# Performance work log

Hardware: AMD Instinct MI355X
Metric: run time of the kernel (lower is better)

The kernel has to match this reference:

```python
import jax, jax.numpy as jnp
import numpy as np

B, T1, T2, D = 8, 2048, 2048, 256


def setup_inputs() -> dict:
    key = jax.random.key(0)
    k1, k2 = jax.random.split(key)
    s1 = jax.random.normal(k1, (B, T1, D), dtype=jnp.float32)
    s2 = jax.random.normal(k2, (B, T2, D), dtype=jnp.float32)
    return {"s1": s1, "s2": s2}


def reference(s1, s2):
    # similarity: [B, t1, t2]
    s = jnp.einsum('bid,bjd->bij', s1, s2)
    # softmax over t2, replace NaNs with 0 (matches masked_fill_(w != w, 0))
    w = jax.nn.softmax(s, axis=2)
    w = jnp.where(jnp.isnan(w), jnp.zeros((), w.dtype), w)
    # one-hot of argmax over t2 (vectorized replacement of the double loop)
    idx = jnp.argmax(w, axis=2)                       # [B, t1]
    a_weight_like = jax.nn.one_hot(idx, s2.shape[1], dtype=s1.dtype)  # [B, t1, t2]
    # gather the argmax rows of s2: [B, t1, D]
    u_tile = jnp.einsum('bij,bjd->bid', a_weight_like, s2)
    return (u_tile, a_weight_like)
```

## Files before the change

kernel.cpp:

```cpp
#include <hip/hip_runtime.h>
#include <math.h>

typedef unsigned short ushort_t;

constexpr int BB = 8, T1 = 2048, T2 = 2048, D = 256;
constexpr float MARGIN = 4e-3f;

constexpr size_t OFF_QC    = 0;
constexpr size_t OFF_QUEUE = 64;
constexpr size_t OFF_PART  = 131072;
constexpr size_t OFF_S1P   = (size_t)2 << 20;
constexpr size_t SZ_PACK   = (size_t)BB * 128 * 8 * 2 * 64 * 16;
constexpr size_t OFF_S2P   = OFF_S1P + SZ_PACK;
constexpr size_t WS_NEEDED = OFF_S2P + SZ_PACK;

typedef __attribute__((ext_vector_type(8))) __bf16 bf16x8;
typedef __attribute__((ext_vector_type(4))) float  f32x4;

__device__ __forceinline__ unsigned f2bf(float x) {
    unsigned u = __float_as_uint(x);
    return (u + 0x7fffu + ((u >> 16) & 1u)) >> 16;
}
__device__ __forceinline__ float bf2f(unsigned h) { return __uint_as_float(h << 16); }

__global__ __launch_bounds__(256) void k_convert(
    const float* __restrict__ s1, const float* __restrict__ s2,
    ushort_t* __restrict__ s1p, ushort_t* __restrict__ s2p)
{
    __shared__ __align__(16) ushort_t L[16384];
    const int bx = blockIdx.x;
    const int tensor = bx >> 9, b = (bx >> 6) & 7, rt = bx & 63;
    const float* src = (tensor ? s2 : s1) + ((size_t)b * 2048 + rt * 32) * 256;
    ushort_t* dst = (tensor ? s2p : s1p) + (size_t)(b * 128 + rt * 2) * 8192;
    const int t = threadIdx.x;
#pragma unroll
    for (int i = 0; i < 8; ++i) {
        int f = i * 256 + t, rw = f >> 6, c4 = f & 63, k0 = c4 * 4;
        float4 v = *(const float4*)(src + rw * 256 + k0);
        unsigned hx = f2bf(v.x), hy = f2bf(v.y), hz = f2bf(v.z), hw = f2bf(v.w);
        ushort4 hi = make_ushort4((ushort_t)hx, (ushort_t)hy, (ushort_t)hz, (ushort_t)hw);
        ushort4 lo = make_ushort4((ushort_t)f2bf(v.x - bf2f(hx)), (ushort_t)f2bf(v.y - bf2f(hy)),
                                  (ushort_t)f2bf(v.z - bf2f(hz)), (ushort_t)f2bf(v.w - bf2f(hw)));
        int tile = rw >> 4, m = rw & 15, g = k0 >> 5;
        int lane = m + 16 * ((k0 >> 3) & 3), i0 = k0 & 7;
        int off = (tile * 8 + g) * 1024 + lane * 8 + i0;
        *(ushort4*)(&L[off])       = hi;
        *(ushort4*)(&L[off + 512]) = lo;
    }
    __syncthreads();
#pragma unroll
    for (int i = 0; i < 8; ++i) {
        int cidx = i * 256 + t;
        ((uint4*)dst)[cidx] = ((const uint4*)L)[cidx];
    }
}

__global__ __launch_bounds__(256, 2) void k_score(
    const ushort_t* __restrict__ s1p, const ushort_t* __restrict__ s2p,
    float4* __restrict__ part)
{
    __shared__ __align__(16) ushort_t AL[16 * 512];
    __shared__ __align__(16) ushort_t BL[32 * 512];
    __shared__ float4 mrg[128][2];

    const int bx = blockIdx.x;
    const int b = bx & 7, rt16 = (bx >> 3) & 15, jq = bx >> 7;
    const int t = threadIdx.x, w = t >> 6, l = t & 63;
    const int rh = w >> 1, jw = w & 1;
    const int q = l >> 4, n = l & 15;

    mrg[t >> 1][t & 1] = make_float4(-INFINITY, -INFINITY, __int_as_float(0), 0.f);

    const ushort_t* Abase = s1p + (size_t)(b * 128 + rt16 * 8) * 8192;

    f32x4 acc[4][8];

    for (int jiter = 0; jiter < 2; ++jiter) {
        const ushort_t* Bbase = s2p + (size_t)(b * 128 + jq * 32 + jiter * 16) * 8192;
#pragma unroll
        for (int rtl = 0; rtl < 4; ++rtl)
#pragma unroll
            for (int jt = 0; jt < 8; ++jt)
#pragma unroll
                for (int r = 0; r < 4; ++r) acc[rtl][jt][r] = 0.f;

        for (int g = 0; g < 8; ++g) {
            __syncthreads();
            for (int s = 0; s * 4 < 48; ++s) {
                int c = s * 4 + w;
                uint4 v;
                if (c < 16)
                    v = *(const uint4*)(Abase + (size_t)(c >> 1) * 8192 + g * 1024 + (c & 1) * 512 + l * 8);
                else {
                    int cc = c - 16;
                    v = *(const uint4*)(Bbase + (size_t)(cc >> 1) * 8192 + g * 1024 + (cc & 1) * 512 + l * 8);
                }
                if (c < 16) *(uint4*)(&AL[c * 512 + l * 8]) = v;
                else        *(uint4*)(&BL[(c - 16) * 512 + l * 8]) = v;
            }
            __syncthreads();

            bf16x8 aF[4][2];
#pragma unroll
            for (int rtl = 0; rtl < 4; ++rtl)
#pragma unroll
                for (int lb = 0; lb < 2; ++lb)
                    aF[rtl][lb] = *(const bf16x8*)(&AL[((rh * 4 + rtl) * 2 + lb) * 512 + l * 8]);
#pragma unroll
            for (int jt = 0; jt < 8; ++jt) {
                bf16x8 bh = *(const bf16x8*)(&BL[((jw * 8 + jt) * 2 + 0) * 512 + l * 8]);
                bf16x8 bl = *(const bf16x8*)(&BL[((jw * 8 + jt) * 2 + 1) * 512 + l * 8]);
#pragma unroll
                for (int rtl = 0; rtl < 4; ++rtl) {
                    acc[rtl][jt] = __builtin_amdgcn_mfma_f32_16x16x32_bf16(aF[rtl][0], bh, acc[rtl][jt], 0, 0, 0);
                    acc[rtl][jt] = __builtin_amdgcn_mfma_f32_16x16x32_bf16(aF[rtl][0], bl, acc[rtl][jt], 0, 0, 0);
                    acc[rtl][jt] = __builtin_amdgcn_mfma_f32_16x16x32_bf16(aF[rtl][1], bh, acc[rtl][jt], 0, 0, 0);
                }
            }
        }

#pragma unroll
        for (int rtl = 0; rtl < 4; ++rtl)
#pragma unroll
            for (int reg = 0; reg < 4; ++reg) {
                float v1 = -INFINITY, v2 = -INFINITY; int i1 = 0;
#pragma unroll
                for (int jt = 0; jt < 8; ++jt) {
                    float v = acc[rtl][jt][reg];
                    int j = jq * 512 + jiter * 256 + jw * 128 + jt * 16 + n;
                    if (v > v1)      { v2 = v1; v1 = v; i1 = j; }
                    else if (v > v2) { v2 = v; }
                }
#pragma unroll
                for (int off = 1; off < 16; off <<= 1) {
                    float b1 = __shfl_xor(v1, off);
                    int   bi = __shfl_xor(i1, off);
                    float b2 = __shfl_xor(v2, off);
                    if (b1 > v1 || (b1 == v1 && bi < i1)) { v2 = fmaxf(v1, b2); v1 = b1; i1 = bi; }
                    else                                   { v2 = fmaxf(b1, v2); }
                }
                int rr = rtl * 4 + reg;
                if (n == rr) {
                    int row = rh * 64 + rtl * 16 + q * 4 + reg;
                    float4 cur = mrg[row][jw];
                    int ci = __float_as_int(cur.z);
                    if (v1 > cur.x || (v1 == cur.x && i1 < ci))
                        mrg[row][jw] = make_float4(v1, fmaxf(v2, cur.x), __int_as_float(i1), 0.f);
                    else
                        mrg[row][jw] = make_float4(cur.x, fmaxf(cur.y, v1), cur.z, 0.f);
                }
            }
    }

    __syncthreads();
    if (t < 128) {
        float4 p0 = mrg[t][0], p1 = mrg[t][1];
        int i0 = __float_as_int(p0.z), i1 = __float_as_int(p1.z);
        float v1, v2; int ii;
        if (p1.x > p0.x || (p1.x == p0.x && i1 < i0)) { v1 = p1.x; v2 = fmaxf(p1.y, p0.x); ii = i1; }
        else                                          { v1 = p0.x; v2 = fmaxf(p0.y, p1.x); ii = i0; }
        part[((size_t)b * 2048 + rt16 * 128 + t) * 4 + jq] =
            make_float4(v1, v2, __int_as_float(ii), 0.f);
    }
}

__global__ __launch_bounds__(256) void k_epilogue(
    const float* __restrict__ s2, const float4* __restrict__ part,
    float* __restrict__ u, float* __restrict__ oh,
    int* __restrict__ qcount, int* __restrict__ queue)
{
    __shared__ int idxs[8];
    const int blk = blockIdx.x, t = threadIdx.x;
    const int r0 = blk * 8;
    const int b = r0 >> 11;
    if (t < 32) {
        int rl = t >> 2, p = t & 3;
        float4 pa = part[(size_t)(r0 + rl) * 4 + p];
        float v1 = pa.x, v2 = pa.y; int i1 = __float_as_int(pa.z);
#pragma unroll
        for (int off = 1; off < 4; off <<= 1) {
            float b1 = __shfl_xor(v1, off);
            int   bi = __shfl_xor(i1, off);
            float b2 = __shfl_xor(v2, off);
            if (b1 > v1 || (b1 == v1 && bi < i1)) { v2 = fmaxf(v1, b2); v1 = b1; i1 = bi; }
            else                                   { v2 = fmaxf(b1, v2); }
        }
        if (p == 0) {
            idxs[rl] = i1;
            if ((v1 - v2) < MARGIN) {
                int pos = atomicAdd(qcount, 1);
                if (pos < 16384) queue[pos] = r0 + rl;
            }
        }
    }
    __syncthreads();
    const float* s2b = s2 + (size_t)b * T2 * D;
    float* ub = u + (size_t)r0 * D;
#pragma unroll
    for (int i = 0; i < 2; ++i) {
        int flat = i * 256 + t, rl = flat >> 6, c = flat & 63;
        float4 v = *(const float4*)(s2b + (size_t)idxs[rl] * D + c * 4);
        *(float4*)(ub + (size_t)rl * D + c * 4) = v;
    }
    float* ohb = oh + (size_t)r0 * T2;
#pragma unroll 4
    for (int i = 0; i < 16; ++i) {
        int flat = i * 256 + t, rl = flat >> 9, c4 = flat & 511;
        int base = c4 * 4, id = idxs[rl];
        float4 vv;
        vv.x = (base     == id) ? 1.f : 0.f;
        vv.y = (base + 1 == id) ? 1.f : 0.f;
        vv.z = (base + 2 == id) ? 1.f : 0.f;
        vv.w = (base + 3 == id) ? 1.f : 0.f;
        *(float4*)(ohb + (size_t)rl * T2 + base) = vv;
    }
}

__global__ __launch_bounds__(256) void k_fixup(
    const float* __restrict__ s1, const float* __restrict__ s2,
    float* __restrict__ u, float* __restrict__ oh,
    const int* __restrict__ qcount, const int* __restrict__ queue, int qcap)
{
    __shared__ double s1d[D];
    __shared__ double rv[256];
    __shared__ int    rj[256];
    int nq = *qcount;
    if (nq > qcap) nq = qcap;
    const int t = threadIdx.x;
    for (int qi = blockIdx.x; qi < nq; qi += gridDim.x) {
        int rg = queue[qi];
        int b = rg >> 11, i = rg & (T1 - 1);
        __syncthreads();
        s1d[t] = (double)s1[((size_t)b * T1 + i) * D + t];
        __syncthreads();
        double bv = -INFINITY; int bj = 0;
        for (int jj = 0; jj < T2 / 256; ++jj) {
            int j = t + jj * 256;
            const float* row = s2 + ((size_t)b * T2 + j) * D;
            double s = 0.0;
            for (int k = 0; k < D; ++k) s = fma((double)row[k], s1d[k], s);
            if (s > bv) { bv = s; bj = j; }
        }
        rv[t] = bv; rj[t] = bj;
        __syncthreads();
        for (int stride = 128; stride > 0; stride >>= 1) {
            if (t < stride) {
                double ov = rv[t + stride]; int oj = rj[t + stride];
                if (ov > rv[t] || (ov == rv[t] && oj < rj[t])) { rv[t] = ov; rj[t] = oj; }
            }
            __syncthreads();
        }
        int best = rj[0];
        float* ohrow = oh + ((size_t)b * T1 + i) * T2;
#pragma unroll
        for (int jj = 0; jj < T2 / 256; ++jj) {
            int j = t + jj * 256;
            ohrow[j] = (j == best) ? 1.f : 0.f;
        }
        u[((size_t)b * T1 + i) * D + t] = s2[((size_t)b * T2 + best) * D + t];
    }
}

constexpr int FB_AST = 264, FB_BST = 72;

__global__ __launch_bounds__(512, 2) void k_score_fb(
    const float* __restrict__ s1, const float* __restrict__ s2,
    float* __restrict__ u, float* __restrict__ oh,
    int* __restrict__ qcount, int* __restrict__ queue, int qcap)
{
    __shared__ __align__(16) short Ah[64 * FB_AST];
    __shared__ __align__(16) short Al[64 * FB_AST];
    __shared__ __align__(16) short Bh[256 * FB_BST];
    __shared__ __align__(16) short Bl[256 * FB_BST];
    __shared__ float cv1[64][4], cv2[64][4];
    __shared__ int   ci1[64][4], idx_s[64];

    const int bx = blockIdx.x;
    const int b  = bx & 7;
    const int r0 = (bx >> 3) * 64;
    const float* s1b = s1 + ((size_t)b * T1 + r0) * D;
    const float* s2b = s2 + (size_t)b * T2 * D;

    const int t = threadIdx.x;
    const int w = t >> 6, l = t & 63, q = l >> 4, ln = l & 15;
    const int rh = w >> 2;
    const int jq = w & 3;

    float4 pa[8];
#pragma unroll
    for (int i = 0; i < 8; ++i) {
        int flat = i * 512 + t, row = flat >> 6, f4 = flat & 63;
        pa[i] = *(const float4*)(s1b + row * D + f4 * 4);
    }
    float4 pb[8];
#pragma unroll
    for (int i = 0; i < 8; ++i) {
        int flat = i * 512 + t, jrow = flat >> 4, f4 = flat & 15;
        pb[i] = *(const float4*)(s2b + (size_t)jrow * D + f4 * 4);
    }
#pragma unroll
    for (int i = 0; i < 8; ++i) {
        int flat = i * 512 + t, row = flat >> 6, f4 = flat & 63;
        float4 v = pa[i];
        unsigned hx = f2bf(v.x), hy = f2bf(v.y), hz = f2bf(v.z), hw = f2bf(v.w);
        uint2 hh, ll;
        hh.x = hx | (hy << 16); hh.y = hz | (hw << 16);
        ll.x = f2bf(v.x - bf2f(hx)) | (f2bf(v.y - bf2f(hy)) << 16);
        ll.y = f2bf(v.z - bf2f(hz)) | (f2bf(v.w - bf2f(hw)) << 16);
        *(uint2*)(&Ah[row * FB_AST + f4 * 4]) = hh;
        *(uint2*)(&Al[row * FB_AST + f4 * 4]) = ll;
    }

    float v1[2][4], v2[2][4]; int i1[2][4];
#pragma unroll
    for (int rt = 0; rt < 2; ++rt)
#pragma unroll
        for (int r = 0; r < 4; ++r) { v1[rt][r] = -INFINITY; v2[rt][r] = -INFINITY; i1[rt][r] = 0; }

    f32x4 acc[2][4];

    for (int c = 0; c < 32; ++c) {
        const int iter = c >> 2, kc = c & 3;
        if (kc == 0) {
#pragma unroll
            for (int rt = 0; rt < 2; ++rt)
#pragma unroll
                for (int jt = 0; jt < 4; ++jt)
#pragma unroll
                    for (int r = 0; r < 4; ++r) acc[rt][jt][r] = 0.f;
        }
        __syncthreads();
#pragma unroll
        for (int i = 0; i < 8; ++i) {
            int flat = i * 512 + t, jrow = flat >> 4, f4 = flat & 15;
            float4 v = pb[i];
            unsigned hx = f2bf(v.x), hy = f2bf(v.y), hz = f2bf(v.z), hw = f2bf(v.w);
            uint2 hh, ll;
            hh.x = hx | (hy << 16); hh.y = hz | (hw << 16);
            ll.x = f2bf(v.x - bf2f(hx)) | (f2bf(v.y - bf2f(hy)) << 16);
            ll.y = f2bf(v.z - bf2f(hz)) | (f2bf(v.w - bf2f(hw)) << 16);
            *(uint2*)(&Bh[jrow * FB_BST + f4 * 4]) = hh;
            *(uint2*)(&Bl[jrow * FB_BST + f4 * 4]) = ll;
        }
        if (c < 31) {
            int c2 = c + 1, it2 = c2 >> 2, kc2 = c2 & 3;
#pragma unroll
            for (int i = 0; i < 8; ++i) {
                int flat = i * 512 + t, jrow = flat >> 4, f4 = flat & 15;
                pb[i] = *(const float4*)(s2b + (size_t)(it2 * 256 + jrow) * D + kc2 * 64 + f4 * 4);
            }
        }
        __syncthreads();

#pragma unroll
        for (int ks = 0; ks < 2; ++ks) {
            const int kA = kc * 64 + ks * 32 + q * 8;
            bf16x8 ah[2], al8[2];
#pragma unroll
            for (int rt = 0; rt < 2; ++rt) {
                int off = (rh * 32 + rt * 16 + ln) * FB_AST + kA;
                ah[rt]  = *(const bf16x8*)(&Ah[off]);
                al8[rt] = *(const bf16x8*)(&Al[off]);
            }
#pragma unroll
            for (int jt = 0; jt < 4; ++jt) {
                int boff = (jq * 64 + jt * 16 + ln) * FB_BST + ks * 32 + q * 8;
                bf16x8 bh = *(const bf16x8*)(&Bh[boff]);
                bf16x8 bl = *(const bf16x8*)(&Bl[boff]);
#pragma unroll
                for (int rt = 0; rt < 2; ++rt) {
                    acc[rt][jt] = __builtin_amdgcn_mfma_f32_16x16x32_bf16(ah[rt],  bh, acc[rt][jt], 0, 0, 0);
                    acc[rt][jt] = __builtin_amdgcn_mfma_f32_16x16x32_bf16(ah[rt],  bl, acc[rt][jt], 0, 0, 0);
                    acc[rt][jt] = __builtin_amdgcn_mfma_f32_16x16x32_bf16(al8[rt], bh, acc[rt][jt], 0, 0, 0);
                }
            }
        }

        if (kc == 3) {
#pragma unroll
            for (int rt = 0; rt < 2; ++rt)
#pragma unroll
                for (int jt = 0; jt < 4; ++jt)
#pragma unroll
                    for (int r = 0; r < 4; ++r) {
                        float val = acc[rt][jt][r];
                        int j = iter * 256 + jq * 64 + jt * 16 + ln;
                        if (val > v1[rt][r]) { v2[rt][r] = v1[rt][r]; v1[rt][r] = val; i1[rt][r] = j; }
                        else if (val > v2[rt][r]) v2[rt][r] = val;
                    }
        }
    }

#pragma unroll
    for (int rt = 0; rt < 2; ++rt)
#pragma unroll
        for (int r = 0; r < 4; ++r) {
            float a1 = v1[rt][r], a2 = v2[rt][r]; int ai = i1[rt][r];
#pragma unroll
            for (int off = 1; off < 16; off <<= 1) {
                float b1 = __shfl_xor(a1, off);
                int   bi = __shfl_xor(ai, off);
                float b2 = __shfl_xor(a2, off);
                if (b1 > a1 || (b1 == a1 && bi < ai)) { a2 = fmaxf(a1, b2); a1 = b1; ai = bi; }
                else                                   { a2 = fmaxf(b1, a2); }
            }
            if (ln == 0) {
                int row = rh * 32 + rt * 16 + q * 4 + r;
                cv1[row][jq] = a1; cv2[row][jq] = a2; ci1[row][jq] = ai;
            }
        }
    __syncthreads();

    if (t < 64) {
        float V1 = cv1[t][0], V2 = cv2[t][0]; int I = ci1[t][0];
#pragma unroll
        for (int h = 1; h < 4; ++h) {
            float c1 = cv1[t][h], c2 = cv2[t][h]; int ci = ci1[t][h];
            if (c1 > V1 || (c1 == V1 && ci < I)) { V2 = fmaxf(V1, c2); V1 = c1; I = ci; }
            else                                  { V2 = fmaxf(V2, c1); }
        }
        idx_s[t] = I;
        if (qcap > 0 && (V1 - V2) < MARGIN) {
            int pos = atomicAdd(qcount, 1);
            if (pos < qcap) queue[pos] = b * T1 + r0 + t;
        }
    }
    __syncthreads();

    float* ub = u + ((size_t)b * T1 + r0) * D;
#pragma unroll
    for (int i = 0; i < 8; ++i) {
        int flat = i * 512 + t, row = flat >> 6, f4 = flat & 63;
        float4 v = *(const float4*)(s2b + (size_t)idx_s[row] * D + f4 * 4);
        *(float4*)(ub + (size_t)row * D + f4 * 4) = v;
    }
    float* ohb = oh + ((size_t)b * T1 + r0) * T2;
#pragma unroll 4
    for (int i = 0; i < 64; ++i) {
        int flat = i * 512 + t, row = flat >> 9, f4 = flat & 511;
        int base = f4 * 4, id = idx_s[row];
        float4 vv;
        vv.x = (base     == id) ? 1.f : 0.f;
        vv.y = (base + 1 == id) ? 1.f : 0.f;
        vv.z = (base + 2 == id) ? 1.f : 0.f;
        vv.w = (base + 3 == id) ? 1.f : 0.f;
        *(float4*)(ohb + (size_t)row * T2 + base) = vv;
    }
}

extern "C" void kernel_launch(void* const* d_in, const int* in_sizes, int n_in,
                              void* d_out, int out_size, void* d_ws, size_t ws_size,
                              hipStream_t stream)
{
    const float* s1 = (const float*)d_in[0];
    const float* s2 = (const float*)d_in[1];
    float* u  = (float*)d_out;
    float* oh = u + (size_t)BB * T1 * D;
    char* ws = (char*)d_ws;

    if (ws_size >= WS_NEEDED) {
        int*      qc    = (int*)(ws + OFF_QC);
        int*      queue = (int*)(ws + OFF_QUEUE);
        float4*   part  = (float4*)(ws + OFF_PART);
        ushort_t* s1p   = (ushort_t*)(ws + OFF_S1P);
        ushort_t* s2p   = (ushort_t*)(ws + OFF_S2P);
        hipMemsetAsync(ws + OFF_QC, 0, 16, stream);
        k_convert<<<dim3(1024), dim3(256), 0, stream>>>(s1, s2, s1p, s2p);
        k_score<<<dim3(512), dim3(256), 0, stream>>>(s1p, s2p, part);
        k_epilogue<<<dim3(2048), dim3(256), 0, stream>>>(s2, part, u, oh, qc, queue);
        k_fixup<<<dim3(128), dim3(256), 0, stream>>>(s1, s2, u, oh, qc, queue, 16384);
    } else {
        int  qcap   = 0;
        int* qcount = nullptr;
        int* queue  = nullptr;
        if (ws_size >= 256) {
            qcount = (int*)d_ws;
            queue  = (int*)d_ws + 4;
            size_t cap = (ws_size - 16) / sizeof(int);
            qcap = (int)(cap > (size_t)(BB * T1) ? (size_t)(BB * T1) : cap);
            hipMemsetAsync(d_ws, 0, 16, stream);
        }
        k_score_fb<<<dim3(BB * (T1 / 64)), dim3(512), 0, stream>>>(
            s1, s2, u, oh, qcount, queue, qcap);
        if (qcap > 0)
            k_fixup<<<dim3(64), dim3(256), 0, stream>>>(
                s1, s2, u, oh, qcount, queue, qcap);
    }
}
```

Before: 312.8 us.

## Load MFMA fragments directly from global memory instead of staging through LDS

The score kernel no longer stages A and B tiles into shared memory with two barriers per k-step. Each wave now reads its bf16 fragments straight from the pre-packed global buffers, relying on L2/L1 caching for reuse between waves. This drops LDS traffic and barrier stalls, but each A tile is now fetched by two waves and each B tile by two waves from global/cache. Global load latency is also exposed unless the compiler overlaps it with the MFMAs.

```diff
diff --git a/kernel.cpp b/kernel.cpp
--- a/kernel.cpp
+++ b/kernel.cpp
@@ -59,8 +59,6 @@
     const ushort_t* __restrict__ s1p, const ushort_t* __restrict__ s2p,
     float4* __restrict__ part)
 {
-    __shared__ __align__(16) ushort_t AL[16 * 512];
-    __shared__ __align__(16) ushort_t BL[32 * 512];
     __shared__ float4 mrg[128][2];
 
     const int bx = blockIdx.x;
@@ -70,13 +68,15 @@
     const int q = l >> 4, n = l & 15;
 
     mrg[t >> 1][t & 1] = make_float4(-INFINITY, -INFINITY, __int_as_float(0), 0.f);
-
-    const ushort_t* Abase = s1p + (size_t)(b * 128 + rt16 * 8) * 8192;
+    __syncthreads();
+
+    const ushort_t* Aw = s1p + (size_t)(b * 128 + rt16 * 8 + rh * 4) * 8192 + l * 8;
 
     f32x4 acc[4][8];
 
     for (int jiter = 0; jiter < 2; ++jiter) {
-        const ushort_t* Bbase = s2p + (size_t)(b * 128 + jq * 32 + jiter * 16) * 8192;
+        const ushort_t* Bw = s2p + (size_t)(b * 128 + jq * 32 + jiter * 16 + jw * 8) * 8192 + l * 8;
+
 #pragma unroll
         for (int rtl = 0; rtl < 4; ++rtl)
 #pragma unroll
@@ -84,32 +84,20 @@
 #pragma unroll
                 for (int r = 0; r < 4; ++r) acc[rtl][jt][r] = 0.f;
 
+#pragma unroll 1
         for (int g = 0; g < 8; ++g) {
-            __syncthreads();
-            for (int s = 0; s * 4 < 48; ++s) {
-                int c = s * 4 + w;
-                uint4 v;
-                if (c < 16)
-                    v = *(const uint4*)(Abase + (size_t)(c >> 1) * 8192 + g * 1024 + (c & 1) * 512 + l * 8);
-                else {
-                    int cc = c - 16;
-                    v = *(const uint4*)(Bbase + (size_t)(cc >> 1) * 8192 + g * 1024 + (cc & 1) * 512 + l * 8);
-                }
-                if (c < 16) *(uint4*)(&AL[c * 512 + l * 8]) = v;
-                else        *(uint4*)(&BL[(c - 16) * 512 + l * 8]) = v;
-            }
-            __syncthreads();
-
+            const ushort_t* Ag = Aw + g * 1024;
+            const ushort_t* Bg = Bw + g * 1024;
             bf16x8 aF[4][2];
 #pragma unroll
-            for (int rtl = 0; rtl < 4; ++rtl)
-#pragma unroll
-                for (int lb = 0; lb < 2; ++lb)
-                    aF[rtl][lb] = *(const bf16x8*)(&AL[((rh * 4 + rtl) * 2 + lb) * 512 + l * 8]);
+            for (int rtl = 0; rtl < 4; ++rtl) {
+                aF[rtl][0] = *(const bf16x8*)(Ag + (size_t)rtl * 8192);
+                aF[rtl][1] = *(const bf16x8*)(Ag + (size_t)rtl * 8192 + 512);
+            }
 #pragma unroll
             for (int jt = 0; jt < 8; ++jt) {
-                bf16x8 bh = *(const bf16x8*)(&BL[((jw * 8 + jt) * 2 + 0) * 512 + l * 8]);
-                bf16x8 bl = *(const bf16x8*)(&BL[((jw * 8 + jt) * 2 + 1) * 512 + l * 8]);
+                bf16x8 bh = *(const bf16x8*)(Bg + (size_t)jt * 8192);
+                bf16x8 bl = *(const bf16x8*)(Bg + (size_t)jt * 8192 + 512);
 #pragma unroll
                 for (int rtl = 0; rtl < 4; ++rtl) {
                     acc[rtl][jt] = __builtin_amdgcn_mfma_f32_16x16x32_bf16(aF[rtl][0], bh, acc[rtl][jt], 0, 0, 0);
```

Measured after the change: 306.9 us. No clear change (-1.9%).
